# Performance work log

Measured on AMD Instinct MI355X. Metric: run time of the kernel, lower is better.

## Reference

```python
import jax, jax.numpy as jnp
import numpy as np

INPUT_SIZE = 968
HIDDEN = 128
ESP = 1e-6


def _gru_scan(xp, w_hh, b_hh):
    # xp: [T, B, 3H] precomputed input projections; returns [T, B, H]
    B = xp.shape[1]
    h0 = jnp.zeros((B, HIDDEN), dtype=xp.dtype)

    def step(h, xp_t):
        gi_r, gi_z, gi_n = jnp.split(xp_t, 3, axis=-1)
        gh = h @ w_hh.T + b_hh
        gh_r, gh_z, gh_n = jnp.split(gh, 3, axis=-1)
        r = jax.nn.sigmoid(gi_r + gh_r)
        z = jax.nn.sigmoid(gi_z + gh_z)
        n = jnp.tanh(gi_n + r * gh_n)
        h_new = (1.0 - z) * n + z * h
        return h_new, h_new

    _, hs = jax.lax.scan(step, h0, xp)
    return hs


def _bigru_ln(x, w_ih_f, w_hh_f, b_ih_f, b_hh_f,
              w_ih_b, w_hh_b, b_ih_b, b_hh_b, ln_w, ln_b):
    # x: [B, T, D] (batch_first)
    # precompute input projections as one big GEMM per direction
    xp_f = jnp.einsum('btd,gd->btg', x, w_ih_f) + b_ih_f  # [B,T,3H]
    xp_b = jnp.einsum('btd,gd->btg', x, w_ih_b) + b_ih_b
    xp_f = jnp.swapaxes(xp_f, 0, 1)  # [T,B,3H]
    xp_b = jnp.swapaxes(xp_b, 0, 1)[::-1]  # reversed time for backward dir

    h_f = _gru_scan(xp_f, w_hh_f, b_hh_f)          # [T,B,H]
    h_b = _gru_scan(xp_b, w_hh_b, b_hh_b)[::-1]    # [T,B,H], un-reverse

    out = jnp.concatenate([h_f, h_b], axis=-1)     # [T,B,2H]
    out = jnp.swapaxes(out, 0, 1)                  # [B,T,2H]

    # LayerNormal: uses unbiased std (torch.std default, ddof=1), clamped
    mu = jnp.mean(out, axis=-1, keepdims=True)
    sigma = jnp.std(out, axis=-1, keepdims=True, ddof=1)
    sigma = jnp.maximum(sigma, ESP)
    return (out - mu) / sigma * ln_w + ln_b


def setup_inputs() -> dict:
    key = jax.random.key(0)
    ks = jax.random.split(key, 10)
    B, T = 64, 512
    s_ih = 1.0 / np.sqrt(HIDDEN)
    u = lambda k, shape: jax.random.uniform(k, shape, jnp.float32, -s_ih, s_ih)
    return {
        'x': jax.random.normal(ks[0], (B, T, INPUT_SIZE), jnp.float32),
        'w_ih_f': u(ks[1], (3 * HIDDEN, INPUT_SIZE)),
        'w_hh_f': u(ks[2], (3 * HIDDEN, HIDDEN)),
        'b_ih_f': u(ks[3], (3 * HIDDEN,)),
        'b_hh_f': u(ks[4], (3 * HIDDEN,)),
        'w_ih_b': u(ks[5], (3 * HIDDEN, INPUT_SIZE)),
        'w_hh_b': u(ks[6], (3 * HIDDEN, HIDDEN)),
        'b_ih_b': u(ks[7], (3 * HIDDEN,)),
        'b_hh_b': u(ks[8], (3 * HIDDEN,)),
        'ln_w': jnp.ones((2 * HIDDEN,), jnp.float32),
        'ln_b': jnp.zeros((2 * HIDDEN,), jnp.float32),
    }


def reference(x, w_ih_f, w_hh_f, b_ih_f, b_hh_f,
              w_ih_b, w_hh_b, b_ih_b, b_hh_b, ln_w, ln_b):
    return _bigru_ln(x, w_ih_f, w_hh_f, b_ih_f, b_hh_f,
                     w_ih_b, w_hh_b, b_ih_b, b_hh_b, ln_w, ln_b)
```

## Files before the change

kernel.cpp:

```cpp
#include <hip/hip_runtime.h>
#include <stdint.h>


#define LOG2E 1.4426950408889634f
#define TT 512
#define D_IN 968
#define KP 992
#define NOUT 768
#define HID 128

typedef __attribute__((ext_vector_type(8))) short short8;
typedef __attribute__((ext_vector_type(4))) float f32x4;
typedef __attribute__((ext_vector_type(4))) unsigned int u32x4;
typedef __attribute__((ext_vector_type(2))) unsigned int u32x2;

__device__ __forceinline__ unsigned short f2bf(float f) {
  unsigned u = __builtin_bit_cast(unsigned, f);
  u += 0x7FFFu + ((u >> 16) & 1u);
  return (unsigned short)(u >> 16);
}
__device__ __forceinline__ unsigned pack2bf(float a, float b) {
  return (unsigned)f2bf(a) | ((unsigned)f2bf(b) << 16);
}
__device__ __forceinline__ float exp2_(float x) { return __builtin_amdgcn_exp2f(x); }
__device__ __forceinline__ float rcp_(float x)  { return __builtin_amdgcn_rcpf(x); }

__device__ __forceinline__ void async_load16(const void* g, void* l) {
  __builtin_amdgcn_global_load_lds(
      (const __attribute__((address_space(1))) unsigned int*)g,
      (__attribute__((address_space(3))) unsigned int*)l, 16, 0, 0);
}

#define WIH_BYTES (NOUT * KP * 2)
#define WHH_BYTES (NOUT * HID * 2)
#define BIAS_BYTES (NOUT * 4)
#define XP_OFF (WIH_BYTES + WHH_BYTES + BIAS_BYTES)

__global__ __launch_bounds__(256) void k0_convert(
    const float* __restrict__ wihf, const float* __restrict__ whhf,
    const float* __restrict__ bihf, const float* __restrict__ wihb,
    const float* __restrict__ whhb, const float* __restrict__ bihb,
    unsigned short* __restrict__ wih16, unsigned short* __restrict__ whh16,
    float* __restrict__ bias_s) {
  int blk = blockIdx.x, tid = threadIdx.x;
  if (blk < NOUT) {
    int n = blk;
    float sc = ((n % 384) < 256) ? LOG2E : 2.0f * LOG2E;
    const float* src = (n < 384) ? (wihf + (long)n * D_IN) : (wihb + (long)(n - 384) * D_IN);
    for (int c = 0; c < 4; c++) {
      int k = c * 256 + tid;
      if (k < KP) {
        float v = (k < D_IN) ? src[k] * sc : 0.0f;
        wih16[(long)n * KP + k] = f2bf(v);
      }
    }
  } else if (blk < NOUT + 96) {
    int e0 = ((blk - NOUT) * 256 + tid) * 4;
    for (int i = 0; i < 4; i++) {
      int e = e0 + i;
      int m = e >> 7, k = e & 127;
      float sc = ((m % 384) < 256) ? LOG2E : 2.0f * LOG2E;
      float v = (m < 384) ? whhf[m * HID + k] : whhb[(m - 384) * HID + k];
      whh16[e] = f2bf(v * sc);
    }
  } else {
    for (int c = 0; c < 3; c++) {
      int n = c * 256 + tid;
      if (n < NOUT) {
        float sc = ((n % 384) < 256) ? LOG2E : 2.0f * LOG2E;
        bias_s[n] = ((n < 384) ? bihf[n] : bihb[n - 384]) * sc;
      }
    }
  }
}

#define AS_STRIDE 40

__global__ __launch_bounds__(256, 2) void k1_gemm(
    const float* __restrict__ X, const unsigned short* __restrict__ W,
    const float* __restrict__ bias_s, float* __restrict__ XP) {
  __shared__ unsigned short As[128 * AS_STRIDE];
  __shared__ unsigned short Bs[128 * 32];

  const int tid = threadIdx.x;
  const int lane = tid & 63, w = tid >> 6;
  const int q = lane >> 4, l15 = lane & 15;
  const int wr = w >> 1, wc = w & 1;
  const int nt = blockIdx.x;
  const int mt = blockIdx.y;
  const long R0 = (long)mt * 128;
  const int C0 = nt * 128;
  const int ar = tid >> 1, ahf = tid & 1;

  f32x4 acc[4][4];
#pragma unroll
  for (int i = 0; i < 4; i++)
#pragma unroll
    for (int j = 0; j < 4; j++) acc[i][j] = {0.f, 0.f, 0.f, 0.f};

  const float* arow = X + (R0 + ar) * D_IN;

  for (int it = 0; it < 31; it++) {
    int k0 = it * 32;
    unsigned pk[8];
#pragma unroll
    for (int c = 0; c < 4; c++) {
      int kc = k0 + ahf * 16 + c * 4;
      kc = (kc <= 964) ? kc : 964;
      f32x4 v = *(const f32x4*)(arow + kc);
      pk[c * 2 + 0] = pack2bf(v.x, v.y);
      pk[c * 2 + 1] = pack2bf(v.z, v.w);
    }
    unsigned short* adst = &As[ar * AS_STRIDE + ahf * 16];
    u32x4 w0 = {pk[0], pk[1], pk[2], pk[3]};
    u32x4 w1 = {pk[4], pk[5], pk[6], pk[7]};
    *(u32x4*)adst = w0;
    *(u32x4*)(adst + 8) = w1;
#pragma unroll
    for (int c = 0; c < 2; c++) {
      int idx = c * 256 + w * 64 + lane;
      int brow = idx >> 2, koff = (idx & 3) * 8;
      const unsigned short* gsrc = W + (long)(C0 + brow) * KP + k0 + koff;
      async_load16(gsrc, ((char*)Bs) + (c * 256 + w * 64) * 16);
    }
    __syncthreads();
    short8 af[4], bf[4];
#pragma unroll
    for (int i = 0; i < 4; i++) {
      int m = wr * 64 + i * 16 + l15;
      af[i] = *(const short8*)&As[m * AS_STRIDE + q * 8];
    }
#pragma unroll
    for (int j = 0; j < 4; j++) {
      int n = wc * 64 + j * 16 + l15;
      bf[j] = *(const short8*)&Bs[n * 32 + q * 8];
    }
#pragma unroll
    for (int i = 0; i < 4; i++)
#pragma unroll
      for (int j = 0; j < 4; j++)
        acc[i][j] = __builtin_amdgcn_mfma_f32_16x16x32_bf16(af[i], bf[j], acc[i][j], 0, 0, 0);
    __syncthreads();
  }
  float bv[4];
#pragma unroll
  for (int j = 0; j < 4; j++) bv[j] = bias_s[C0 + wc * 64 + j * 16 + l15];
#pragma unroll
  for (int i = 0; i < 4; i++)
#pragma unroll
    for (int j = 0; j < 4; j++) {
      int col = C0 + wc * 64 + j * 16 + l15;
      long Rb = R0 + wr * 64 + i * 16 + q * 4;
#pragma unroll
      for (int r = 0; r < 4; r++)
        XP[(Rb + r) * NOUT + col] = acc[i][j][r] + bv[j];
    }
}

#define GI_STRIDE 52

__global__ __launch_bounds__(512) void k2_gru(
    const unsigned short* __restrict__ WHH, const float* __restrict__ XP,
    const float* __restrict__ bhh_f, const float* __restrict__ bhh_b,
    float* __restrict__ OUT) {
  __shared__ unsigned short Hl[2][16 * 128];
  __shared__ float GIl[8][16 * GI_STRIDE];

  const int tid = threadIdx.x;
  const int lane = tid & 63, w = tid >> 6;
  const int q = lane >> 4, b = lane & 15;
  const int dir = blockIdx.x & 1, bg = blockIdx.x >> 1;
  const int j0 = w * 16 + q * 4;

  for (int i = tid; i < 2 * 16 * 128; i += 512) ((unsigned short*)Hl)[i] = 0;

  short8 afr[3][4];
#pragma unroll
  for (int g = 0; g < 3; g++)
#pragma unroll
    for (int kt = 0; kt < 4; kt++) {
      int row = dir * 384 + g * 128 + w * 16 + b;
      afr[g][kt] = *(const short8*)(WHH + (long)row * HID + kt * 32 + q * 8);
    }
  const float* bhh = dir ? bhh_b : bhh_f;
  f32x4 bh[3];
#pragma unroll
  for (int g = 0; g < 3; g++) {
    f32x4 t = *(const f32x4*)(bhh + g * 128 + j0);
    float sc = (g < 2) ? LOG2E : 2.0f * LOG2E;
    bh[g] = t * sc;
  }

  const int lb = lane >> 2, lc = lane & 3;
  const long gi_base = (long)(bg * 16 + lb) * TT * NOUT + dir * 384 + w * 16 + lc * 4;
  float* giw = &GIl[w][lb * GI_STRIDE + lc * 4];
  const float* gir = &GIl[w][b * GI_STRIDE];
  const long out_base = (long)(bg * 16 + b) * TT * 256 + dir * 128 + j0;

  {
    int td0 = dir ? (TT - 1) : 0;
    const float* gb = XP + gi_base + (long)td0 * NOUT;
    f32x4 g0 = *(const f32x4*)(gb);
    f32x4 g1 = *(const f32x4*)(gb + 128);
    f32x4 g2 = *(const f32x4*)(gb + 256);
    *(f32x4*)(giw + 0) = g0;
    *(f32x4*)(giw + 16) = g1;
    *(f32x4*)(giw + 32) = g2;
  }
  f32x4 h = {0.f, 0.f, 0.f, 0.f};
  __syncthreads();

  for (int t = 0; t < TT; t++) {
    const int cur = t & 1, nxt = cur ^ 1;
    const int td = dir ? (TT - 1 - t) : t;
    const int tn = (t + 1 < TT) ? t + 1 : t;
    const int tdn = dir ? (TT - 1 - tn) : tn;

    short8 bfr[4];
#pragma unroll
    for (int kt = 0; kt < 4; kt++) {
      int ch = ((kt * 4 + q) ^ (b & 7)) * 8;
      bfr[kt] = *(const short8*)&Hl[cur][b * 128 + ch];
    }
    f32x4 accR = {0.f, 0.f, 0.f, 0.f};
    f32x4 accZ = {0.f, 0.f, 0.f, 0.f};
    f32x4 accN = {0.f, 0.f, 0.f, 0.f};
#pragma unroll
    for (int kt = 0; kt < 4; kt++) {
      accR = __builtin_amdgcn_mfma_f32_16x16x32_bf16(afr[0][kt], bfr[kt], accR, 0, 0, 0);
      accZ = __builtin_amdgcn_mfma_f32_16x16x32_bf16(afr[1][kt], bfr[kt], accZ, 0, 0, 0);
      accN = __builtin_amdgcn_mfma_f32_16x16x32_bf16(afr[2][kt], bfr[kt], accN, 0, 0, 0);
    }
    const float* gb = XP + gi_base + (long)tdn * NOUT;
    f32x4 gp0 = *(const f32x4*)(gb);
    f32x4 gp1 = *(const f32x4*)(gb + 128);
    f32x4 gp2 = *(const f32x4*)(gb + 256);

    f32x4 gr = *(const f32x4*)(gir + 0 + q * 4);
    f32x4 gz = *(const f32x4*)(gir + 16 + q * 4);
    f32x4 gn = *(const f32x4*)(gir + 32 + q * 4);
    f32x4 hnew;
#pragma unroll
    for (int i = 0; i < 4; i++) {
      float pr = gr[i] + accR[i] + bh[0][i];
      float pz = gz[i] + accZ[i] + bh[1][i];
      float r = rcp_(1.0f + exp2_(-pr));
      float z = rcp_(1.0f + exp2_(-pz));
      float pn = gn[i] + r * (accN[i] + bh[2][i]);
      float n = 1.0f - 2.0f * rcp_(exp2_(pn) + 1.0f);
      hnew[i] = n + z * (h[i] - n);
    }
    h = hnew;
    {
      int ch = ((j0 >> 3) ^ (b & 7)) * 8 + (j0 & 7);
      u32x2 hv = {pack2bf(hnew[0], hnew[1]), pack2bf(hnew[2], hnew[3])};
      *(u32x2*)&Hl[nxt][b * 128 + ch] = hv;
    }
    *(f32x4*)(OUT + out_base + (long)td * 256) = hnew;
    *(f32x4*)(giw + 0) = gp0;
    *(f32x4*)(giw + 16) = gp1;
    *(f32x4*)(giw + 32) = gp2;
    __syncthreads();
  }
}

__global__ __launch_bounds__(256) void k3_ln(float* __restrict__ OUT,
                                             const float* __restrict__ lnw,
                                             const float* __restrict__ lnb) {
  const int tid = threadIdx.x, lane = tid & 63, w = tid >> 6;
  const long row = (long)blockIdx.x * 4 + w;
  float* p = OUT + row * 256 + lane * 4;
  f32x4 x = *(const f32x4*)p;
  float s = x[0] + x[1] + x[2] + x[3];
  float s2 = x[0] * x[0] + x[1] * x[1] + x[2] * x[2] + x[3] * x[3];
#pragma unroll
  for (int m = 1; m < 64; m <<= 1) {
    s += __shfl_xor(s, m, 64);
    s2 += __shfl_xor(s2, m, 64);
  }
  float mu = s * (1.0f / 256.0f);
  float var = (s2 - s * mu) * (1.0f / 255.0f);
  var = fmaxf(var, 0.0f);
  float sig = fmaxf(sqrtf(var), 1e-6f);
  float inv = 1.0f / sig;
  f32x4 wv = *(const f32x4*)(lnw + lane * 4);
  f32x4 bv = *(const f32x4*)(lnb + lane * 4);
  f32x4 y;
#pragma unroll
  for (int i = 0; i < 4; i++) y[i] = (x[i] - mu) * inv * wv[i] + bv[i];
  *(f32x4*)p = y;
}

extern "C" void kernel_launch(void* const* d_in, const int* in_sizes, int n_in,
                              void* d_out, int out_size, void* d_ws, size_t ws_size,
                              hipStream_t stream) {
  const float* x = (const float*)d_in[0];
  const float* wihf = (const float*)d_in[1];
  const float* whhf = (const float*)d_in[2];
  const float* bihf = (const float*)d_in[3];
  const float* bhhf = (const float*)d_in[4];
  const float* wihb = (const float*)d_in[5];
  const float* whhb = (const float*)d_in[6];
  const float* bihb = (const float*)d_in[7];
  const float* bhhb = (const float*)d_in[8];
  const float* lnw = (const float*)d_in[9];
  const float* lnb = (const float*)d_in[10];

  char* ws = (char*)d_ws;
  unsigned short* wih16 = (unsigned short*)ws;
  unsigned short* whh16 = (unsigned short*)(ws + WIH_BYTES);
  float* bias_s = (float*)(ws + WIH_BYTES + WHH_BYTES);
  float* xp = (float*)(ws + XP_OFF);
  float* out = (float*)d_out;

  hipLaunchKernelGGL(k0_convert, dim3(768 + 96 + 1), dim3(256), 0, stream,
                     wihf, whhf, bihf, wihb, whhb, bihb, wih16, whh16, bias_s);
  hipLaunchKernelGGL(k1_gemm, dim3(6, 256), dim3(256), 0, stream, x, wih16, bias_s, xp);
  hipLaunchKernelGGL(k2_gru, dim3(8), dim3(512), 0, stream, whh16, xp, bhhf, bhhb, out);
  hipLaunchKernelGGL(k3_ln, dim3(8192), dim3(256), 0, stream, out, lnw, lnb);
}
```

Baseline: 755.2 us.

## Pre-convert X to bf16 for async GEMM loads and deepen GRU input prefetch

Result: faster. 678.2 us (-10.2%).

```diff
diff --git a/kernel.cpp b/kernel.cpp
--- a/kernel.cpp
+++ b/kernel.cpp
@@ -31,10 +31,29 @@
       (__attribute__((address_space(3))) unsigned int*)l, 16, 0, 0);
 }
 
+__device__ __forceinline__ void wg_barrier_lds() {
+  asm volatile("s_waitcnt lgkmcnt(0)\n\ts_barrier" ::: "memory");
+}
+
 #define WIH_BYTES (NOUT * KP * 2)
 #define WHH_BYTES (NOUT * HID * 2)
-#define BIAS_BYTES (NOUT * 4)
-#define XP_OFF (WIH_BYTES + WHH_BYTES + BIAS_BYTES)
+#define BIAS_BYTES 3072
+#define BASE_OFF (WIH_BYTES + WHH_BYTES + BIAS_BYTES)
+#define XBF_BYTES ((size_t)32768 * KP * 2)
+#define XP_BYTES ((size_t)32768 * NOUT * 4)
+
+__global__ __launch_bounds__(256) void kx_convert(const float* __restrict__ X,
+                                                  unsigned short* __restrict__ Xb) {
+  const long row = blockIdx.x;
+  const int t = threadIdx.x;
+  if (t < 242) {
+    f32x4 v = *(const f32x4*)(X + row * D_IN + t * 4);
+    u32x2 p = {pack2bf(v.x, v.y), pack2bf(v.z, v.w)};
+    *(u32x2*)(Xb + row * KP + t * 4) = p;
+  } else if (t < 248) {
+    *(u32x2*)(Xb + row * KP + t * 4) = (u32x2){0, 0};
+  }
+}
 
 __global__ __launch_bounds__(256) void k0_convert(
     const float* __restrict__ wihf, const float* __restrict__ whhf,
@@ -74,12 +93,10 @@
   }
 }
 
-#define AS_STRIDE 40
-
-__global__ __launch_bounds__(256, 2) void k1_gemm(
-    const float* __restrict__ X, const unsigned short* __restrict__ W,
+__global__ __launch_bounds__(256, 2) void k1_gemm_fast(
+    const unsigned short* __restrict__ Xb, const unsigned short* __restrict__ W,
     const float* __restrict__ bias_s, float* __restrict__ XP) {
-  __shared__ unsigned short As[128 * AS_STRIDE];
+  __shared__ unsigned short As[128 * 32];
   __shared__ unsigned short Bs[128 * 32];
 
   const int tid = threadIdx.x;
@@ -90,16 +107,74 @@
   const int mt = blockIdx.y;
   const long R0 = (long)mt * 128;
   const int C0 = nt * 128;
+
+  f32x4 acc[4][4];
+#pragma unroll
+  for (int i = 0; i < 4; i++)
+#pragma unroll
+    for (int j = 0; j < 4; j++) acc[i][j] = {0.f, 0.f, 0.f, 0.f};
+
+  for (int it = 0; it < 31; it++) {
+    const int k0 = it * 32;
+#pragma unroll
+    for (int c = 0; c < 2; c++) {
+      int idx = c * 256 + w * 64 + lane;
+      int row = idx >> 2, koff = (idx & 3) * 8;
+      async_load16(Xb + (R0 + row) * KP + k0 + koff,
+                   ((char*)As) + (c * 256 + w * 64) * 16);
+      async_load16(W + (long)(C0 + row) * KP + k0 + koff,
+                   ((char*)Bs) + (c * 256 + w * 64) * 16);
+    }
+    __syncthreads();
+    short8 af[4], bf[4];
+#pragma unroll
+    for (int i = 0; i < 4; i++)
+      af[i] = *(const short8*)&As[(wr * 64 + i * 16 + l15) * 32 + q * 8];
+#pragma unroll
+    for (int j = 0; j < 4; j++)
+      bf[j] = *(const short8*)&Bs[(wc * 64 + j * 16 + l15) * 32 + q * 8];
+#pragma unroll
+    for (int i = 0; i < 4; i++)
+#pragma unroll
+      for (int j = 0; j < 4; j++)
+        acc[i][j] = __builtin_amdgcn_mfma_f32_16x16x32_bf16(af[i], bf[j], acc[i][j], 0, 0, 0);
+    __syncthreads();
+  }
+  float bv[4];
+#pragma unroll
+  for (int j = 0; j < 4; j++) bv[j] = bias_s[C0 + wc * 64 + j * 16 + l15];
+#pragma unroll
+  for (int i = 0; i < 4; i++)
+#pragma unroll
+    for (int j = 0; j < 4; j++) {
+      int col = C0 + wc * 64 + j * 16 + l15;
+      long Rb = R0 + wr * 64 + i * 16 + q * 4;
+#pragma unroll
+      for (int r = 0; r < 4; r++)
+        XP[(Rb + r) * NOUT + col] = acc[i][j][r] + bv[j];
+    }
+}
+
+#define AS_STRIDE 40
+__global__ __launch_bounds__(256, 2) void k1_gemm_slow(
+    const float* __restrict__ X, const unsigned short* __restrict__ W,
+    const float* __restrict__ bias_s, float* __restrict__ XP) {
+  __shared__ unsigned short As[128 * AS_STRIDE];
+  __shared__ unsigned short Bs[128 * 32];
+  const int tid = threadIdx.x;
+  const int lane = tid & 63, w = tid >> 6;
+  const int q = lane >> 4, l15 = lane & 15;
+  const int wr = w >> 1, wc = w & 1;
+  const int nt = blockIdx.x, mt = blockIdx.y;
+  const long R0 = (long)mt * 128;
+  const int C0 = nt * 128;
   const int ar = tid >> 1, ahf = tid & 1;
-
   f32x4 acc[4][4];
 #pragma unroll
   for (int i = 0; i < 4; i++)
 #pragma unroll
     for (int j = 0; j < 4; j++) acc[i][j] = {0.f, 0.f, 0.f, 0.f};
-
   const float* arow = X + (R0 + ar) * D_IN;
-
   for (int it = 0; it < 31; it++) {
     int k0 = it * 32;
     unsigned pk[8];
@@ -112,29 +187,23 @@
       pk[c * 2 + 1] = pack2bf(v.z, v.w);
     }
     unsigned short* adst = &As[ar * AS_STRIDE + ahf * 16];
-    u32x4 w0 = {pk[0], pk[1], pk[2], pk[3]};
-    u32x4 w1 = {pk[4], pk[5], pk[6], pk[7]};
-    *(u32x4*)adst = w0;
-    *(u32x4*)(adst + 8) = w1;
+    *(u32x4*)adst = (u32x4){pk[0], pk[1], pk[2], pk[3]};
+    *(u32x4*)(adst + 8) = (u32x4){pk[4], pk[5], pk[6], pk[7]};
 #pragma unroll
     for (int c = 0; c < 2; c++) {
       int idx = c * 256 + w * 64 + lane;
       int brow = idx >> 2, koff = (idx & 3) * 8;
-      const unsigned short* gsrc = W + (long)(C0 + brow) * KP + k0 + koff;
-      async_load16(gsrc, ((char*)Bs) + (c * 256 + w * 64) * 16);
+      async_load16(W + (long)(C0 + brow) * KP + k0 + koff,
+                   ((char*)Bs) + (c * 256 + w * 64) * 16);
     }
     __syncthreads();
     short8 af[4], bf[4];
 #pragma unroll
-    for (int i = 0; i < 4; i++) {
-      int m = wr * 64 + i * 16 + l15;
-      af[i] = *(const short8*)&As[m * AS_STRIDE + q * 8];
-    }
-#pragma unroll
-    for (int j = 0; j < 4; j++) {
-      int n = wc * 64 + j * 16 + l15;
-      bf[j] = *(const short8*)&Bs[n * 32 + q * 8];
-    }
+    for (int i = 0; i < 4; i++)
+      af[i] = *(const short8*)&As[(wr * 64 + i * 16 + l15) * AS_STRIDE + q * 8];
+#pragma unroll
+    for (int j = 0; j < 4; j++)
+      bf[j] = *(const short8*)&Bs[(wc * 64 + j * 16 + l15) * 32 + q * 8];
 #pragma unroll
     for (int i = 0; i < 4; i++)
 #pragma unroll
@@ -164,7 +233,7 @@
     const float* __restrict__ bhh_f, const float* __restrict__ bhh_b,
     float* __restrict__ OUT) {
   __shared__ unsigned short Hl[2][16 * 128];
-  __shared__ float GIl[8][16 * GI_STRIDE];
+  __shared__ float GIl[2][8][16 * GI_STRIDE];
 
   const int tid = threadIdx.x;
   const int lane = tid & 63, w = tid >> 6;
@@ -187,25 +256,29 @@
 #pragma unroll
   for (int g = 0; g < 3; g++) {
     f32x4 t = *(const f32x4*)(bhh + g * 128 + j0);
-    float sc = (g < 2) ? LOG2E : 2.0f * LOG2E;
-    bh[g] = t * sc;
+    bh[g] = t * ((g < 2) ? LOG2E : 2.0f * LOG2E);
   }
 
   const int lb = lane >> 2, lc = lane & 3;
   const long gi_base = (long)(bg * 16 + lb) * TT * NOUT + dir * 384 + w * 16 + lc * 4;
-  float* giw = &GIl[w][lb * GI_STRIDE + lc * 4];
-  const float* gir = &GIl[w][b * GI_STRIDE];
   const long out_base = (long)(bg * 16 + b) * TT * 256 + dir * 128 + j0;
 
+  f32x4 gp0, gp1, gp2;
   {
-    int td0 = dir ? (TT - 1) : 0;
+    const int td0 = dir ? (TT - 1) : 0;
     const float* gb = XP + gi_base + (long)td0 * NOUT;
-    f32x4 g0 = *(const f32x4*)(gb);
-    f32x4 g1 = *(const f32x4*)(gb + 128);
-    f32x4 g2 = *(const f32x4*)(gb + 256);
-    *(f32x4*)(giw + 0) = g0;
-    *(f32x4*)(giw + 16) = g1;
-    *(f32x4*)(giw + 32) = g2;
+    f32x4 a0 = *(const f32x4*)(gb);
+    f32x4 a1 = *(const f32x4*)(gb + 128);
+    f32x4 a2 = *(const f32x4*)(gb + 256);
+    float* giw0 = &GIl[0][w][lb * GI_STRIDE + lc * 4];
+    *(f32x4*)(giw0 + 0) = a0;
+    *(f32x4*)(giw0 + 16) = a1;
+    *(f32x4*)(giw0 + 32) = a2;
+    const int td1 = dir ? (TT - 2) : 1;
+    const float* gb1 = XP + gi_base + (long)td1 * NOUT;
+    gp0 = *(const f32x4*)(gb1);
+    gp1 = *(const f32x4*)(gb1 + 128);
+    gp2 = *(const f32x4*)(gb1 + 256);
   }
   f32x4 h = {0.f, 0.f, 0.f, 0.f};
   __syncthreads();
@@ -213,14 +286,26 @@
   for (int t = 0; t < TT; t++) {
     const int cur = t & 1, nxt = cur ^ 1;
     const int td = dir ? (TT - 1 - t) : t;
-    const int tn = (t + 1 < TT) ? t + 1 : t;
-    const int tdn = dir ? (TT - 1 - tn) : tn;
 
     short8 bfr[4];
 #pragma unroll
     for (int kt = 0; kt < 4; kt++) {
       int ch = ((kt * 4 + q) ^ (b & 7)) * 8;
       bfr[kt] = *(const short8*)&Hl[cur][b * 128 + ch];
+    }
+    {
+      float* giw = &GIl[nxt][w][lb * GI_STRIDE + lc * 4];
+      *(f32x4*)(giw + 0) = gp0;
+      *(f32x4*)(giw + 16) = gp1;
+      *(f32x4*)(giw + 32) = gp2;
+    }
+    {
+      int tn2 = (t + 2 < TT) ? t + 2 : TT - 1;
+      int tdn2 = dir ? (TT - 1 - tn2) : tn2;
+      const float* gb = XP + gi_base + (long)tdn2 * NOUT;
+      gp0 = *(const f32x4*)(gb);
+      gp1 = *(const f32x4*)(gb + 128);
+      gp2 = *(const f32x4*)(gb + 256);
     }
     f32x4 accR = {0.f, 0.f, 0.f, 0.f};
     f32x4 accZ = {0.f, 0.f, 0.f, 0.f};
@@ -231,11 +316,7 @@
       accZ = __builtin_amdgcn_mfma_f32_16x16x32_bf16(afr[1][kt], bfr[kt], accZ, 0, 0, 0);
       accN = __builtin_amdgcn_mfma_f32_16x16x32_bf16(afr[2][kt], bfr[kt], accN, 0, 0, 0);
     }
-    const float* gb = XP + gi_base + (long)tdn * NOUT;
-    f32x4 gp0 = *(const f32x4*)(gb);
-    f32x4 gp1 = *(const f32x4*)(gb + 128);
-    f32x4 gp2 = *(const f32x4*)(gb + 256);
-
+    const float* gir = &GIl[cur][w][b * GI_STRIDE];
     f32x4 gr = *(const f32x4*)(gir + 0 + q * 4);
     f32x4 gz = *(const f32x4*)(gir + 16 + q * 4);
     f32x4 gn = *(const f32x4*)(gir + 32 + q * 4);
@@ -257,10 +338,7 @@
       *(u32x2*)&Hl[nxt][b * 128 + ch] = hv;
     }
     *(f32x4*)(OUT + out_base + (long)td * 256) = hnew;
-    *(f32x4*)(giw + 0) = gp0;
-    *(f32x4*)(giw + 16) = gp1;
-    *(f32x4*)(giw + 32) = gp2;
-    __syncthreads();
+    wg_barrier_lds();
   }
 }
 
@@ -310,12 +388,25 @@
   unsigned short* wih16 = (unsigned short*)ws;
   unsigned short* whh16 = (unsigned short*)(ws + WIH_BYTES);
   float* bias_s = (float*)(ws + WIH_BYTES + WHH_BYTES);
-  float* xp = (float*)(ws + XP_OFF);
   float* out = (float*)d_out;
+
+  const size_t need_fast = (size_t)BASE_OFF + XBF_BYTES + XP_BYTES;
 
   hipLaunchKernelGGL(k0_convert, dim3(768 + 96 + 1), dim3(256), 0, stream,
                      wihf, whhf, bihf, wihb, whhb, bihb, wih16, whh16, bias_s);
-  hipLaunchKernelGGL(k1_gemm, dim3(6, 256), dim3(256), 0, stream, x, wih16, bias_s, xp);
+
+  float* xp;
+  if (ws_size >= need_fast) {
+    unsigned short* xbf = (unsigned short*)(ws + BASE_OFF);
+    xp = (float*)(ws + BASE_OFF + XBF_BYTES);
+    hipLaunchKernelGGL(kx_convert, dim3(32768), dim3(256), 0, stream, x, xbf);
+    hipLaunchKernelGGL(k1_gemm_fast, dim3(6, 256), dim3(256), 0, stream,
+                       xbf, wih16, bias_s, xp);
+  } else {
+    xp = (float*)(ws + BASE_OFF);
+    hipLaunchKernelGGL(k1_gemm_slow, dim3(6, 256), dim3(256), 0, stream,
+                       x, wih16, bias_s, xp);
+  }
   hipLaunchKernelGGL(k2_gru, dim3(8), dim3(512), 0, stream, whh16, xp, bhhf, bhhb, out);
   hipLaunchKernelGGL(k3_ln, dim3(8192), dim3(256), 0, stream, out, lnw, lnb);
 }
```
